# Kernel optimization log

Measured on AMD Instinct MI355X. Metric: run time of the kernel, lower is better.

Reference implementation:

```python
import jax, jax.numpy as jnp
import numpy as np

B_, N, C, H, WS, NW = 2048, 49, 384, 12, 7, 64
D = C // H  # head_dim = 32
SCALE = D ** -0.5


def _relative_position_index(ws=WS):
    coords = np.stack(np.meshgrid(np.arange(ws), np.arange(ws), indexing='ij'))  # [2,ws,ws]
    flat = coords.reshape(2, -1)                         # [2, N]
    rel = flat[:, :, None] - flat[:, None, :]            # [2, N, N]
    rel = rel.transpose(1, 2, 0)                         # [N, N, 2]
    rel[..., 0] += ws - 1
    rel[..., 1] += ws - 1
    rel[..., 0] *= 2 * ws - 1
    return rel.sum(-1).astype(np.int32)                  # [N, N]


def setup_inputs() -> dict:
    key = jax.random.key(0)
    ks = jax.random.split(key, 9)
    return {
        'x1': jax.random.normal(ks[0], (B_, N, C), jnp.float32),
        'x2': jax.random.normal(ks[1], (B_, N, C), jnp.float32),
        'mask1': jax.random.normal(ks[2], (NW, N, N), jnp.float32),
        'mask2': jax.random.normal(ks[3], (NW, N, N), jnp.float32),
        'w_qkv': jax.random.normal(ks[4], (C, 3 * C), jnp.float32) * 0.02,
        'b_qkv': jax.random.normal(ks[5], (3 * C,), jnp.float32) * 0.02,
        'w_proj': jax.random.normal(ks[6], (C, C), jnp.float32) * 0.02,
        'b_proj': jax.random.normal(ks[7], (C,), jnp.float32) * 0.02,
        'rpb_table': jax.random.normal(ks[8], ((2 * WS - 1) ** 2, H), jnp.float32) * 0.02,
        'rel_index': jnp.asarray(_relative_position_index()),
    }


def _qkv(x, w_qkv, b_qkv):
    # x: [B_, N, C] -> q,k,v each [B_, H, N, D]
    qkv = (x @ w_qkv + b_qkv).reshape(B_, N, 3, H, D).transpose(2, 0, 3, 1, 4)
    return qkv[0], qkv[1], qkv[2]


def reference(x1, x2, mask1, mask2, w_qkv, b_qkv, w_proj, b_proj, rpb_table, rel_index):
    # relative position bias: [H, N, N]
    rpb = rpb_table[rel_index.reshape(-1)].reshape(N, N, H).transpose(2, 0, 1)

    q1, k1, v1 = _qkv(x1, w_qkv, b_qkv)
    _, k2, v2 = _qkv(x2, w_qkv, b_qkv)
    q1s = q1 * SCALE

    attn1 = jnp.einsum('bhnd,bhmd->bhnm', q1s, k1) + rpb[None]
    attn2 = jnp.einsum('bhnd,bhmd->bhnm', q1s, k2) + rpb[None]  # note: q1, per source

    # shifted-window mask add: [B_//nW, nW, H, N, N] + mask[None, :, None]
    attn1 = (attn1.reshape(B_ // NW, NW, H, N, N) + mask1[None, :, None]).reshape(B_, H, N, N)
    attn2 = (attn2.reshape(B_ // NW, NW, H, N, N) + mask2[None, :, None]).reshape(B_, H, N, N)

    attn = jax.nn.softmax(jnp.concatenate([attn1, attn2], axis=1), axis=-1)  # [B_, 2H, N, N]

    v = jnp.concatenate([v1, v2], axis=1)  # [B_, 2H, N, D]
    out = jnp.einsum('bhnm,bhmd->bhnd', attn, v)
    weights = out.transpose(0, 2, 1, 3).reshape(B_, N, 2 * C)
    x = weights[:, :, :C] @ w_proj + b_proj
    return x, weights
```

## Files before the change

### kernel.cpp

```cpp
#include <hip/hip_runtime.h>

typedef unsigned short u16;
typedef unsigned int u32;
typedef __attribute__((ext_vector_type(8))) short short8;
typedef __attribute__((ext_vector_type(4))) float f32x4;

#define NB 2048
#define NTOK 49
#define CH 384
#define NH 12
#define HD 32
#define SCALE_Q 0.17677669529663687f

__device__ __forceinline__ u16 f2bf(float f) {
  u32 u = __float_as_uint(f);
  u += 0x7fffu + ((u >> 16) & 1u);
  return (u16)(u >> 16);
}
__device__ __forceinline__ float bf2f(u16 h) { return __uint_as_float(((u32)h) << 16); }
__device__ __forceinline__ u32 pk2(float a, float b) { return (u32)f2bf(a) | ((u32)f2bf(b) << 16); }

__device__ __forceinline__ void gload16(const u16* g, u16* l) {
  __builtin_amdgcn_global_load_lds(
      (const __attribute__((address_space(1))) u32*)g,
      (__attribute__((address_space(3))) u32*)l,
      16, 0, 0);
}

__global__ void prep_kernel(const float* __restrict__ w_qkv, const float* __restrict__ w_proj,
                            const float* __restrict__ rpb_table, const int* __restrict__ rel_index,
                            u16* __restrict__ wqkvT, u16* __restrict__ wprojT, float* __restrict__ rpb)
{
  int idx = blockIdx.x * 256 + threadIdx.x;
  if (idx < 1152 * 384) {
    int n = idx / 384, k = idx - n * 384;
    wqkvT[idx] = f2bf(w_qkv[(size_t)k * 1152 + n]);
  } else if (idx < 1152 * 384 + 384 * 384) {
    int i2 = idx - 1152 * 384;
    int n = i2 / 384, k = i2 - n * 384;
    wprojT[i2] = f2bf(w_proj[(size_t)k * 384 + n]);
  } else if (idx < 1152 * 384 + 384 * 384 + 12 * 2401) {
    int i3 = idx - (1152 * 384 + 384 * 384);
    int hh = i3 / 2401, r = i3 - hh * 2401;
    rpb[i3] = rpb_table[(size_t)rel_index[r] * 12 + hh];
  }
}

__global__ __launch_bounds__(256) void conv_bf16(const float* __restrict__ x1, const float* __restrict__ x2,
                                                 u16* __restrict__ xb1, u16* __restrict__ xb2)
{
  const size_t i = ((size_t)blockIdx.x * 256 + threadIdx.x) * 8;
  float4 a = *reinterpret_cast<const float4*>(x1 + i);
  float4 b = *reinterpret_cast<const float4*>(x1 + i + 4);
  uint4 o;
  o.x = pk2(a.x, a.y); o.y = pk2(a.z, a.w); o.z = pk2(b.x, b.y); o.w = pk2(b.z, b.w);
  *reinterpret_cast<uint4*>(xb1 + i) = o;
  a = *reinterpret_cast<const float4*>(x2 + i);
  b = *reinterpret_cast<const float4*>(x2 + i + 4);
  o.x = pk2(a.x, a.y); o.y = pk2(a.z, a.w); o.z = pk2(b.x, b.y); o.w = pk2(b.z, b.w);
  *reinterpret_cast<uint4*>(xb2 + i) = o;
}

__global__ __launch_bounds__(256) void gemm_qkv(
    const u16* __restrict__ xb1, const u16* __restrict__ xb2,
    const u16* __restrict__ wT, const float* __restrict__ bias,
    u16* __restrict__ q1, u16* __restrict__ k1, u16* __restrict__ v1,
    u16* __restrict__ k2, u16* __restrict__ v2)
{
  __shared__ __align__(16) u16 smem[2][2][8192];
  u16* Cs = &smem[0][0][0];

  const int bid0 = blockIdx.x;
  const int lin = (bid0 & 7) * 1470 + (bid0 >> 3);
  const int mt = lin / 15;
  const int nt = lin - mt * 15;

  const bool isx2 = nt >= 9;
  const u16* __restrict__ X = isx2 ? xb2 : xb1;
  const int colbase = isx2 ? 384 + (nt - 9) * 128 : nt * 128;
  const int m0 = mt * 128;
  const int tid = threadIdx.x;
  const int lane = tid & 63, wv = tid >> 6;
  const int wr = wv >> 1, wc = wv & 1;
  const int l15 = lane & 15, l4 = lane >> 4;

  f32x4 acc[4][4] = {};

  const u16* ga = X + (size_t)(m0 + l15) * CH + l4 * 8;
  const u16* gb = wT + (size_t)(colbase + l15) * CH + l4 * 8;
  int goff[4];
#pragma unroll
  for (int u = 0; u < 4; ++u) {
    const int g = u * 4 + wv, i = g >> 1, ks = g & 1;
    goff[u] = i * 16 * CH + ks * 32;
  }

  auto stage = [&](int bs, int kk) {
#pragma unroll
    for (int u = 0; u < 4; ++u) {
      const int g = u * 4 + wv;
      gload16(ga + kk + goff[u], &smem[bs][0][g * 512]);
      gload16(gb + kk + goff[u], &smem[bs][1][g * 512]);
    }
  };

  stage(0, 0);
  stage(1, 64);

#pragma unroll
  for (int k = 0; k < 6; ++k) {
    if (k < 5) asm volatile("s_waitcnt vmcnt(8)" ::: "memory");
    else       asm volatile("s_waitcnt vmcnt(0)" ::: "memory");
    __builtin_amdgcn_s_barrier();
    __builtin_amdgcn_sched_barrier(0);
    const int cb = k & 1;
#pragma unroll
    for (int ks = 0; ks < 2; ++ks) {
      short8 af[4], bfr[4];
#pragma unroll
      for (int i = 0; i < 4; ++i)
        af[i] = *reinterpret_cast<const short8*>(&smem[cb][0][((wr * 4 + i) * 2 + ks) * 512 + lane * 8]);
#pragma unroll
      for (int j = 0; j < 4; ++j)
        bfr[j] = *reinterpret_cast<const short8*>(&smem[cb][1][((wc * 4 + j) * 2 + ks) * 512 + lane * 8]);
#pragma unroll
      for (int i = 0; i < 4; ++i)
#pragma unroll
        for (int j = 0; j < 4; ++j)
          acc[i][j] = __builtin_amdgcn_mfma_f32_16x16x32_bf16(af[i], bfr[j], acc[i][j], 0, 0, 0);
    }
    asm volatile("s_waitcnt lgkmcnt(0)" ::: "memory");
    __builtin_amdgcn_s_barrier();
    __builtin_amdgcn_sched_barrier(0);
    if (k + 2 < 6) stage(cb, (k + 2) * 64);
  }

#pragma unroll
  for (int j = 0; j < 4; ++j) {
    const int colL = wc * 64 + j * 16 + l15;
    const int gcol = colbase + colL;
    const float bb = bias[gcol];
    const float scl = (gcol < 384) ? SCALE_Q : 1.0f;
#pragma unroll
    for (int i = 0; i < 4; ++i)
#pragma unroll
      for (int r = 0; r < 4; ++r) {
        const int row = wr * 64 + i * 16 + l4 * 4 + r;
        Cs[row * 152 + (colL ^ (((row >> 2) & 3) << 3))] = f2bf((acc[i][j][r] + bb) * scl);
      }
  }
  __syncthreads();

  u16* dst;
  int tb;
  if (colbase < 384)      { dst = q1;              tb = colbase; }
  else if (colbase < 768) { dst = isx2 ? k2 : k1;  tb = colbase - 384; }
  else                    { dst = isx2 ? v2 : v1;  tb = colbase - 768; }

#pragma unroll
  for (int u = 0; u < 8; ++u) {
    const int pc = tid + u * 256;
    const int row = pc >> 4, pp = pc & 15;
    const uint4 val = *reinterpret_cast<const uint4*>(&Cs[row * 152 + ((pp ^ ((row >> 2) & 3)) << 3)]);
    const int gm = m0 + row;
    const int b = gm / 49, tok = gm - b * 49;
    const int cm = tb + pp * 8;
    const int h = cm >> 5, d0 = cm & 31;
    *reinterpret_cast<uint4*>(&dst[(((size_t)b * NH + h) * NTOK + tok) * HD + d0]) = val;
  }
}

__global__ __launch_bounds__(256) void attn_kernel(
    const u16* __restrict__ q1, const u16* __restrict__ k1, const u16* __restrict__ v1,
    const u16* __restrict__ k2, const u16* __restrict__ v2,
    const float* __restrict__ mask1, const float* __restrict__ mask2,
    const float* __restrict__ rpb, float* __restrict__ outw)
{
  __shared__ __align__(16) u16 VT[2][32][72];
  __shared__ __align__(16) u16 Pl[64][72];

  const int h = blockIdx.x, b = blockIdx.y;
  const int tid = threadIdx.x;
  const int lane = tid & 63, mt = tid >> 6;
  const int l15 = lane & 15, l4 = lane >> 4;
  const size_t base = ((size_t)b * NH + h) * 1568;

  for (int e = tid; e < 1568; e += 256) {
    int tok = e >> 5, d = e & 31;
    VT[0][d][tok] = v1[base + e];
    VT[1][d][tok] = v2[base + e];
  }
  for (int e = tid; e < 2 * 32 * 15; e += 256) {
    int p = (e >= 480) ? 1 : 0;
    int e2 = e - p * 480;
    int d = e2 / 15, j = 49 + (e2 - d * 15);
    VT[p][d][j] = 0;
  }

  const short8 aq = *reinterpret_cast<const short8*>(&q1[base + (mt * 16 + l15) * 32 + l4 * 8]);

  __syncthreads();

  const int wb = b & 63;
  const float* rp = rpb + h * 2401;
  const size_t obase = (size_t)b * (NTOK * 768) + (size_t)h * 32;

#pragma unroll
  for (int p = 0; p < 2; ++p) {
    const u16* __restrict__ kp = p ? k2 : k1;
    const float* __restrict__ msk = (p ? mask2 : mask1) + (size_t)wb * 2401;

    f32x4 s[4];
#pragma unroll
    for (int n = 0; n < 4; ++n) {
      short8 bk = *reinterpret_cast<const short8*>(&kp[base + (n * 16 + l15) * 32 + l4 * 8]);
      s[n] = __builtin_amdgcn_mfma_f32_16x16x32_bf16(aq, bk, (f32x4){0.f, 0.f, 0.f, 0.f}, 0, 0, 0);
    }

#pragma unroll
    for (int r = 0; r < 4; ++r) {
      const int i = mt * 16 + l4 * 4 + r;
#pragma unroll
      for (int n = 0; n < 4; ++n) {
        const int j = n * 16 + l15;
        float v = s[n][r];
        if (j < 49) { if (i < 49) v += rp[i * 49 + j] + msk[i * 49 + j]; }
        else v = -1e30f;
        s[n][r] = v;
      }
    }

#pragma unroll
    for (int r = 0; r < 4; ++r) {
      float mx = fmaxf(fmaxf(s[0][r], s[1][r]), fmaxf(s[2][r], s[3][r]));
      mx = fmaxf(mx, __shfl_xor(mx, 1));
      mx = fmaxf(mx, __shfl_xor(mx, 2));
      mx = fmaxf(mx, __shfl_xor(mx, 4));
      mx = fmaxf(mx, __shfl_xor(mx, 8));
      float e0 = __expf(s[0][r] - mx), e1 = __expf(s[1][r] - mx);
      float e2 = __expf(s[2][r] - mx), e3 = __expf(s[3][r] - mx);
      float sm = (e0 + e1) + (e2 + e3);
      sm += __shfl_xor(sm, 1);
      sm += __shfl_xor(sm, 2);
      sm += __shfl_xor(sm, 4);
      sm += __shfl_xor(sm, 8);
      const float si = 1.f / sm;
      s[0][r] = e0 * si; s[1][r] = e1 * si; s[2][r] = e2 * si; s[3][r] = e3 * si;
    }

#pragma unroll
    for (int n = 0; n < 4; ++n)
#pragma unroll
      for (int r = 0; r < 4; ++r)
        Pl[mt * 16 + l4 * 4 + r][n * 16 + l15] = f2bf(s[n][r]);

    f32x4 o[2] = {};
#pragma unroll
    for (int kt = 0; kt < 2; ++kt) {
      short8 ap = *reinterpret_cast<const short8*>(&Pl[mt * 16 + l15][kt * 32 + l4 * 8]);
#pragma unroll
      for (int n2 = 0; n2 < 2; ++n2) {
        short8 bvf = *reinterpret_cast<const short8*>(&VT[p][n2 * 16 + l15][kt * 32 + l4 * 8]);
        o[n2] = __builtin_amdgcn_mfma_f32_16x16x32_bf16(ap, bvf, o[n2], 0, 0, 0);
      }
    }

#pragma unroll
    for (int n2 = 0; n2 < 2; ++n2)
#pragma unroll
      for (int r = 0; r < 4; ++r) {
        const int i = mt * 16 + l4 * 4 + r;
        if (i < 49)
          outw[obase + (size_t)i * 768 + p * 384 + n2 * 16 + l15] = o[n2][r];
      }
  }
}

__global__ __launch_bounds__(256) void gemm_proj(
    const float* __restrict__ Wsrc, const u16* __restrict__ wT,
    const float* __restrict__ bias, float* __restrict__ outx)
{
  __shared__ __align__(16) u16 smem[2][2][8192];
  const int bid0 = blockIdx.x;
  const int lin = (bid0 & 7) * 294 + (bid0 >> 3);
  const int mt = lin / 3;
  const int nt = lin - mt * 3;

  const int colbase = nt * 128;
  const int m0 = mt * 128;
  const int tid = threadIdx.x;
  const int lane = tid & 63, wv = tid >> 6;
  const int wr = wv >> 1, wc = wv & 1;
  const int l15 = lane & 15, l4 = lane >> 4;

  f32x4 acc[4][4] = {};

  const float* ga = Wsrc + (size_t)(m0 + l15) * 768 + l4 * 4;
  const u16*   gb = wT + (size_t)(colbase + l15) * CH + l4 * 8;
  int aoff[4], boff[4];
#pragma unroll
  for (int u = 0; u < 4; ++u) {
    const int g = u * 4 + wv, i = g >> 1, ks = g & 1;
    aoff[u] = i * 16 * 768 + ks * 32;
    boff[u] = i * 16 * CH + ks * 32;
  }

  float4 areg0[4][2], areg1[4][2];
  auto loadA = [&](float4 (*ar)[2], int kk) {
#pragma unroll
    for (int u = 0; u < 4; ++u)
#pragma unroll
      for (int t = 0; t < 2; ++t)
        ar[u][t] = *reinterpret_cast<const float4*>(ga + kk + aoff[u] + t * 16);
  };
  auto stageB = [&](int bs, int kk) {
#pragma unroll
    for (int u = 0; u < 4; ++u)
      gload16(gb + kk + boff[u], &smem[bs][1][(u * 4 + wv) * 512]);
  };
  auto writeA = [&](float4 (*ar)[2], int bs) {
#pragma unroll
    for (int u = 0; u < 4; ++u) {
      const int g = u * 4 + wv;
#pragma unroll
      for (int t = 0; t < 2; ++t) {
        uint2 pkd;
        pkd.x = pk2(ar[u][t].x, ar[u][t].y);
        pkd.y = pk2(ar[u][t].z, ar[u][t].w);
        *reinterpret_cast<uint2*>(&smem[bs][0][g * 512 + (t * 2 + (l4 >> 1)) * 128 + l15 * 8 + (l4 & 1) * 4]) = pkd;
      }
    }
  };

  loadA(areg0, 0);   stageB(0, 0);
  loadA(areg1, 64);  stageB(1, 64);

#pragma unroll
  for (int k = 0; k < 6; ++k) {
    if (k < 5) asm volatile("s_waitcnt vmcnt(12)" ::: "memory");
    else       asm volatile("s_waitcnt vmcnt(0)" ::: "memory");
    const int cb = k & 1;
    if (cb == 0) writeA(areg0, 0); else writeA(areg1, 1);
    asm volatile("s_waitcnt lgkmcnt(0)" ::: "memory");
    __builtin_amdgcn_s_barrier();
    __builtin_amdgcn_sched_barrier(0);
#pragma unroll
    for (int ks = 0; ks < 2; ++ks) {
      short8 af[4], bfr[4];
#pragma unroll
      for (int i = 0; i < 4; ++i)
        af[i] = *reinterpret_cast<const short8*>(&smem[cb][0][((wr * 4 + i) * 2 + ks) * 512 + lane * 8]);
#pragma unroll
      for (int j = 0; j < 4; ++j)
        bfr[j] = *reinterpret_cast<const short8*>(&smem[cb][1][((wc * 4 + j) * 2 + ks) * 512 + lane * 8]);
#pragma unroll
      for (int i = 0; i < 4; ++i)
#pragma unroll
        for (int j = 0; j < 4; ++j)
          acc[i][j] = __builtin_amdgcn_mfma_f32_16x16x32_bf16(af[i], bfr[j], acc[i][j], 0, 0, 0);
    }
    asm volatile("s_waitcnt lgkmcnt(0)" ::: "memory");
    __builtin_amdgcn_s_barrier();
    __builtin_amdgcn_sched_barrier(0);
    if (k + 2 < 6) {
      if (cb == 0) loadA(areg0, (k + 2) * 64); else loadA(areg1, (k + 2) * 64);
      stageB(cb, (k + 2) * 64);
    }
  }

#pragma unroll
  for (int j = 0; j < 4; ++j) {
    const int col = colbase + wc * 64 + j * 16 + l15;
    const float bb = bias[col];
#pragma unroll
    for (int i = 0; i < 4; ++i) {
#pragma unroll
      for (int r = 0; r < 4; ++r) {
        const int gm = m0 + wr * 64 + i * 16 + l4 * 4 + r;
        outx[(size_t)gm * CH + col] = acc[i][j][r] + bb;
      }
    }
  }
}

extern "C" void kernel_launch(void* const* d_in, const int* in_sizes, int n_in,
                              void* d_out, int out_size, void* d_ws, size_t ws_size,
                              hipStream_t stream) {
  const float* x1        = (const float*)d_in[0];
  const float* x2        = (const float*)d_in[1];
  const float* mask1     = (const float*)d_in[2];
  const float* mask2     = (const float*)d_in[3];
  const float* w_qkv     = (const float*)d_in[4];
  const float* b_qkv     = (const float*)d_in[5];
  const float* w_proj    = (const float*)d_in[6];
  const float* b_proj    = (const float*)d_in[7];
  const float* rpb_table = (const float*)d_in[8];
  const int*   rel_index = (const int*)d_in[9];

  float* outx = (float*)d_out;
  const size_t SZe = (size_t)NB * NH * NTOK * HD;
  float* outw = outx + SZe;

  u16* q1 = (u16*)d_out;
  u16* k1 = q1 + SZe;
  u16* xb1 = (u16*)outw;
  u16* xb2 = xb1 + SZe;

  u16* v1 = (u16*)d_ws;
  u16* k2 = v1 + SZe;
  u16* v2 = k2 + SZe;
  u16* wqkvT  = v2 + SZe;
  u16* wprojT = wqkvT + 1152 * 384;
  float* rpb  = (float*)(wprojT + 384 * 384);

  {
    int total = 1152 * 384 + 384 * 384 + 12 * 2401;
    prep_kernel<<<(total + 255) / 256, 256, 0, stream>>>(w_qkv, w_proj, rpb_table, rel_index,
                                                         wqkvT, wprojT, rpb);
  }
  conv_bf16<<<(int)(SZe / (256 * 8)), 256, 0, stream>>>(x1, x2, xb1, xb2);
  gemm_qkv<<<11760, 256, 0, stream>>>(xb1, xb2, wqkvT, b_qkv, q1, k1, v1, k2, v2);
  attn_kernel<<<dim3(12, 2048), 256, 0, stream>>>(q1, k1, v1, k2, v2, mask1, mask2, rpb, outw);
  gemm_proj<<<2352, 256, 0, stream>>>(outw, wprojT, b_proj, outx);
}
```

Before: 851.1 us.

## Precombine bias+mask table, transpose score MFMA, vectorize V loads in attention

Adds a prep kernel that precomputes rpb+mask for each window, head and branch into a padded 52-wide float table. The attention kernel can then read one float4 per tile instead of two scattered scalar loads per element. The QK MFMA operands are swapped so each lane holds a query row's columns, which cuts the softmax cross-lane shuffles to two per reduction. P is written in packed bf16 pairs in the MFMA operand layout, V is loaded as 16-byte vectors before the LDS transpose, and setprio hints are placed around the MFMAs. The cost is an extra table of about 15MB written and read from global memory.

```diff
diff --git a/kernel.cpp b/kernel.cpp
--- a/kernel.cpp
+++ b/kernel.cpp
@@ -11,6 +11,7 @@
 #define NH 12
 #define HD 32
 #define SCALE_Q 0.17677669529663687f
+#define TABF 1956864
 
 __device__ __forceinline__ u16 f2bf(float f) {
   u32 u = __float_as_uint(f);
@@ -27,9 +28,8 @@
       16, 0, 0);
 }
 
-__global__ void prep_kernel(const float* __restrict__ w_qkv, const float* __restrict__ w_proj,
-                            const float* __restrict__ rpb_table, const int* __restrict__ rel_index,
-                            u16* __restrict__ wqkvT, u16* __restrict__ wprojT, float* __restrict__ rpb)
+__global__ void prep_w(const float* __restrict__ w_qkv, const float* __restrict__ w_proj,
+                       u16* __restrict__ wqkvT, u16* __restrict__ wprojT)
 {
   int idx = blockIdx.x * 256 + threadIdx.x;
   if (idx < 1152 * 384) {
@@ -39,10 +39,23 @@
     int i2 = idx - 1152 * 384;
     int n = i2 / 384, k = i2 - n * 384;
     wprojT[i2] = f2bf(w_proj[(size_t)k * 384 + n]);
-  } else if (idx < 1152 * 384 + 384 * 384 + 12 * 2401) {
-    int i3 = idx - (1152 * 384 + 384 * 384);
-    int hh = i3 / 2401, r = i3 - hh * 2401;
-    rpb[i3] = rpb_table[(size_t)rel_index[r] * 12 + hh];
+  }
+}
+
+__global__ __launch_bounds__(256) void prep_c(const float* __restrict__ rpb_table,
+                                              const int* __restrict__ rel_index,
+                                              const float* __restrict__ mask1,
+                                              const float* __restrict__ mask2,
+                                              float* __restrict__ comb)
+{
+  const int wbh = blockIdx.x;
+  const int wb = wbh / 12, h = wbh - wb * 12;
+  const size_t ob = (size_t)wbh * (49 * 52);
+  for (int r = threadIdx.x; r < 2401; r += 256) {
+    int i = r / 49, j = r - i * 49;
+    float rv = rpb_table[(size_t)rel_index[r] * 12 + h];
+    comb[ob + i * 52 + j]        = rv + mask1[(size_t)wb * 2401 + r];
+    comb[TABF + ob + i * 52 + j] = rv + mask2[(size_t)wb * 2401 + r];
   }
 }
 
@@ -173,22 +186,26 @@
 __global__ __launch_bounds__(256) void attn_kernel(
     const u16* __restrict__ q1, const u16* __restrict__ k1, const u16* __restrict__ v1,
     const u16* __restrict__ k2, const u16* __restrict__ v2,
-    const float* __restrict__ mask1, const float* __restrict__ mask2,
-    const float* __restrict__ rpb, float* __restrict__ outw)
+    const float* __restrict__ comb, float* __restrict__ outw)
 {
   __shared__ __align__(16) u16 VT[2][32][72];
-  __shared__ __align__(16) u16 Pl[64][72];
+  __shared__ __align__(16) u16 Pb[4][2][512];
 
   const int h = blockIdx.x, b = blockIdx.y;
   const int tid = threadIdx.x;
-  const int lane = tid & 63, mt = tid >> 6;
+  const int lane = tid & 63, wt = tid >> 6;
   const int l15 = lane & 15, l4 = lane >> 4;
   const size_t base = ((size_t)b * NH + h) * 1568;
 
-  for (int e = tid; e < 1568; e += 256) {
-    int tok = e >> 5, d = e & 31;
-    VT[0][d][tok] = v1[base + e];
-    VT[1][d][tok] = v2[base + e];
+  for (int e = tid; e < 392; e += 256) {
+    const int p = e >= 196;
+    const int e2 = e - p * 196;
+    const int tok = e2 >> 2, d8 = (e2 & 3) * 8;
+    const u16* src = (p ? v2 : v1) + base + tok * 32 + d8;
+    uint4 val = *reinterpret_cast<const uint4*>(src);
+    const u16* pv = reinterpret_cast<const u16*>(&val);
+#pragma unroll
+    for (int q = 0; q < 8; ++q) VT[p][d8 + q][tok] = pv[q];
   }
   for (int e = tid; e < 2 * 32 * 15; e += 256) {
     int p = (e >= 480) ? 1 : 0;
@@ -197,79 +214,89 @@
     VT[p][d][j] = 0;
   }
 
-  const short8 aq = *reinterpret_cast<const short8*>(&q1[base + (mt * 16 + l15) * 32 + l4 * 8]);
+  const short8 aq = *reinterpret_cast<const short8*>(&q1[base + (wt * 16 + l15) * 32 + l4 * 8]);
 
   __syncthreads();
 
   const int wb = b & 63;
-  const float* rp = rpb + h * 2401;
+  const int irow = wt * 16 + l15;
+  const float* cb0 = comb + ((size_t)(wb * 12 + h) * 49 + (irow < 49 ? irow : 48)) * 52;
   const size_t obase = (size_t)b * (NTOK * 768) + (size_t)h * 32;
 
 #pragma unroll
   for (int p = 0; p < 2; ++p) {
     const u16* __restrict__ kp = p ? k2 : k1;
-    const float* __restrict__ msk = (p ? mask2 : mask1) + (size_t)wb * 2401;
-
-    f32x4 s[4];
-#pragma unroll
-    for (int n = 0; n < 4; ++n) {
-      short8 bk = *reinterpret_cast<const short8*>(&kp[base + (n * 16 + l15) * 32 + l4 * 8]);
-      s[n] = __builtin_amdgcn_mfma_f32_16x16x32_bf16(aq, bk, (f32x4){0.f, 0.f, 0.f, 0.f}, 0, 0, 0);
-    }
-
-#pragma unroll
-    for (int r = 0; r < 4; ++r) {
-      const int i = mt * 16 + l4 * 4 + r;
-#pragma unroll
-      for (int n = 0; n < 4; ++n) {
-        const int j = n * 16 + l15;
-        float v = s[n][r];
-        if (j < 49) { if (i < 49) v += rp[i * 49 + j] + msk[i * 49 + j]; }
-        else v = -1e30f;
-        s[n][r] = v;
-      }
-    }
-
-#pragma unroll
-    for (int r = 0; r < 4; ++r) {
-      float mx = fmaxf(fmaxf(s[0][r], s[1][r]), fmaxf(s[2][r], s[3][r]));
-      mx = fmaxf(mx, __shfl_xor(mx, 1));
-      mx = fmaxf(mx, __shfl_xor(mx, 2));
-      mx = fmaxf(mx, __shfl_xor(mx, 4));
-      mx = fmaxf(mx, __shfl_xor(mx, 8));
-      float e0 = __expf(s[0][r] - mx), e1 = __expf(s[1][r] - mx);
-      float e2 = __expf(s[2][r] - mx), e3 = __expf(s[3][r] - mx);
-      float sm = (e0 + e1) + (e2 + e3);
-      sm += __shfl_xor(sm, 1);
-      sm += __shfl_xor(sm, 2);
-      sm += __shfl_xor(sm, 4);
-      sm += __shfl_xor(sm, 8);
-      const float si = 1.f / sm;
-      s[0][r] = e0 * si; s[1][r] = e1 * si; s[2][r] = e2 * si; s[3][r] = e3 * si;
-    }
-
-#pragma unroll
-    for (int n = 0; n < 4; ++n)
-#pragma unroll
-      for (int r = 0; r < 4; ++r)
-        Pl[mt * 16 + l4 * 4 + r][n * 16 + l15] = f2bf(s[n][r]);
+    const float* cbp = cb0 + (size_t)p * TABF;
+
+    f32x4 st[4];
+    __builtin_amdgcn_s_setprio(1);
+#pragma unroll
+    for (int jt = 0; jt < 4; ++jt) {
+      short8 bk = *reinterpret_cast<const short8*>(&kp[base + (jt * 16 + l15) * 32 + l4 * 8]);
+      st[jt] = __builtin_amdgcn_mfma_f32_16x16x32_bf16(bk, aq, (f32x4){0.f, 0.f, 0.f, 0.f}, 0, 0, 0);
+    }
+    __builtin_amdgcn_s_setprio(0);
+
+#pragma unroll
+    for (int jt = 0; jt < 4; ++jt) {
+      const float4 c = *reinterpret_cast<const float4*>(cbp + jt * 16 + l4 * 4);
+#pragma unroll
+      for (int r = 0; r < 4; ++r) {
+        const int j = jt * 16 + l4 * 4 + r;
+        st[jt][r] = (j < 49) ? st[jt][r] + (&c.x)[r] : -1e30f;
+      }
+    }
+
+    float mx = -1e30f;
+#pragma unroll
+    for (int jt = 0; jt < 4; ++jt)
+#pragma unroll
+      for (int r = 0; r < 4; ++r) mx = fmaxf(mx, st[jt][r]);
+    mx = fmaxf(mx, __shfl_xor(mx, 16));
+    mx = fmaxf(mx, __shfl_xor(mx, 32));
+    float sm = 0.f;
+#pragma unroll
+    for (int jt = 0; jt < 4; ++jt)
+#pragma unroll
+      for (int r = 0; r < 4; ++r) {
+        float e = __expf(st[jt][r] - mx);
+        st[jt][r] = e;
+        sm += e;
+      }
+    sm += __shfl_xor(sm, 16);
+    sm += __shfl_xor(sm, 32);
+    const float si = 1.f / sm;
+
+#pragma unroll
+    for (int jt = 0; jt < 4; ++jt) {
+      const int kt = jt >> 1;
+#pragma unroll
+      for (int r = 0; r < 4; r += 2) {
+        const u32 pkv = pk2(st[jt][r] * si, st[jt][r + 1] * si);
+        const int jrel = (jt & 1) * 16 + l4 * 4 + r;
+        const int off = ((jrel >> 3) << 7) + l15 * 8 + (jrel & 7);
+        *reinterpret_cast<u32*>(&Pb[wt][kt][off]) = pkv;
+      }
+    }
 
     f32x4 o[2] = {};
+    __builtin_amdgcn_s_setprio(1);
 #pragma unroll
     for (int kt = 0; kt < 2; ++kt) {
-      short8 ap = *reinterpret_cast<const short8*>(&Pl[mt * 16 + l15][kt * 32 + l4 * 8]);
+      short8 ap = *reinterpret_cast<const short8*>(&Pb[wt][kt][lane * 8]);
 #pragma unroll
       for (int n2 = 0; n2 < 2; ++n2) {
         short8 bvf = *reinterpret_cast<const short8*>(&VT[p][n2 * 16 + l15][kt * 32 + l4 * 8]);
         o[n2] = __builtin_amdgcn_mfma_f32_16x16x32_bf16(ap, bvf, o[n2], 0, 0, 0);
       }
     }
+    __builtin_amdgcn_s_setprio(0);
 
 #pragma unroll
     for (int n2 = 0; n2 < 2; ++n2)
 #pragma unroll
       for (int r = 0; r < 4; ++r) {
-        const int i = mt * 16 + l4 * 4 + r;
+        const int i = wt * 16 + l4 * 4 + r;
         if (i < 49)
           outw[obase + (size_t)i * 768 + p * 384 + n2 * 16 + l15] = o[n2][r];
       }
@@ -411,15 +438,12 @@
   u16* v2 = k2 + SZe;
   u16* wqkvT  = v2 + SZe;
   u16* wprojT = wqkvT + 1152 * 384;
-  float* rpb  = (float*)(wprojT + 384 * 384);
-
-  {
-    int total = 1152 * 384 + 384 * 384 + 12 * 2401;
-    prep_kernel<<<(total + 255) / 256, 256, 0, stream>>>(w_qkv, w_proj, rpb_table, rel_index,
-                                                         wqkvT, wprojT, rpb);
-  }
+  float* comb = (float*)(wprojT + 384 * 384);
+
+  prep_w<<<2304, 256, 0, stream>>>(w_qkv, w_proj, wqkvT, wprojT);
+  prep_c<<<768, 256, 0, stream>>>(rpb_table, rel_index, mask1, mask2, comb);
   conv_bf16<<<(int)(SZe / (256 * 8)), 256, 0, stream>>>(x1, x2, xb1, xb2);
   gemm_qkv<<<11760, 256, 0, stream>>>(xb1, xb2, wqkvT, b_qkv, q1, k1, v1, k2, v2);
-  attn_kernel<<<dim3(12, 2048), 256, 0, stream>>>(q1, k1, v1, k2, v2, mask1, mask2, rpb, outw);
+  attn_kernel<<<dim3(12, 2048), 256, 0, stream>>>(q1, k1, v1, k2, v2, comb, outw);
   gemm_proj<<<2352, 256, 0, stream>>>(outw, wprojT, b_proj, outx);
 }
```

After: 734.0 us. -13.8%, faster.
